# Performance work log

Hardware: AMD Instinct MI355X
Metric: run time of the kernel (lower is better)

## Reference

```python
import math
import jax, jax.numpy as jnp
import numpy as np

N, L, W = 64, 128, 256          # batch, num windows, window size
D, H, NL = 384, 8, 4            # d_model, heads, transformer layers
DFF = 1536
CH = [1, 4, 16, 64]             # conv channels (multiplier 4)
K = 7                            # conv kernel, pad 3, stride 1; pool k2 s2
LIN_IN = 64 * 32                # cnn_linear_size = 2048


def _pe(l, d):
    pos = np.arange(l)[:, None].astype(np.float32)
    i = np.arange(d // 2)[None, :].astype(np.float32)
    ang = pos / np.power(10000.0, 2.0 * i / d)
    pe = np.zeros((l, d), np.float32)
    pe[:, 0::2] = np.sin(ang)
    pe[:, 1::2] = np.cos(ang)
    return jnp.asarray(pe)


def _conv1d(x, w, b):
    y = jax.lax.conv_general_dilated(x, w, window_strides=(1,), padding=[(3, 3)],
                                     dimension_numbers=('NCH', 'OIH', 'NCH'))
    return y + b[None, :, None]


def _maxpool2(x):
    return jax.lax.reduce_window(x, -jnp.inf, jax.lax.max, (1, 1, 2), (1, 1, 2), 'VALID')


def _ln(x, g, b):
    m = x.mean(-1, keepdims=True)
    v = ((x - m) ** 2).mean(-1, keepdims=True)
    return (x - m) * jax.lax.rsqrt(v + 1e-5) * g + b


def setup_inputs() -> dict:
    key = jax.random.key(0)
    ks = iter(jax.random.split(key, 40))
    s = 0.02
    d = {'x': jax.random.normal(next(ks), (N, L, W), jnp.float32)}
    for i in range(3):
        d[f'conv_w{i}'] = jax.random.normal(next(ks), (CH[i + 1], CH[i], K), jnp.float32) * s
        d[f'conv_b{i}'] = jnp.zeros((CH[i + 1],), jnp.float32)
    d['embed_w'] = jax.random.normal(next(ks), (LIN_IN, D), jnp.float32) * s
    d['embed_b'] = jnp.zeros((D,), jnp.float32)
    for nm, sh in [('Wq', (NL, D, D)), ('Wk', (NL, D, D)), ('Wv', (NL, D, D)), ('Wo', (NL, D, D)),
                   ('W1', (NL, D, DFF)), ('W2', (NL, DFF, D))]:
        d[nm] = jax.random.normal(next(ks), sh, jnp.float32) * s
    for nm, sh in [('bq', (NL, D)), ('bk', (NL, D)), ('bv', (NL, D)), ('bo', (NL, D)),
                   ('b1', (NL, DFF)), ('b2', (NL, D))]:
        d[nm] = jnp.zeros(sh, jnp.float32)
    d['g1'] = jnp.ones((NL, D), jnp.float32); d['be1'] = jnp.zeros((NL, D), jnp.float32)
    d['g2'] = jnp.ones((NL, D), jnp.float32); d['be2'] = jnp.zeros((NL, D), jnp.float32)
    d['cls_w'] = jax.random.normal(next(ks), (D, 1), jnp.float32) * s
    d['cls_b'] = jnp.zeros((1,), jnp.float32)
    return d


def reference(x, conv_w0, conv_b0, conv_w1, conv_b1, conv_w2, conv_b2,
              embed_w, embed_b, Wq, bq, Wk, bk, Wv, bv, Wo, bo,
              W1, b1, W2, b2, g1, be1, g2, be2, cls_w, cls_b):
    n, l, w = x.shape
    # ---- CNN window encoder: each window -> d_model token ----
    h = x.reshape(n * l, 1, w)
    for cw, cb in ((conv_w0, conv_b0), (conv_w1, conv_b1), (conv_w2, conv_b2)):
        h = _maxpool2(jax.nn.relu(_conv1d(h, cw, cb)))
    h = h.reshape(n * l, -1)                      # (N*L, cnn_linear_size)
    h = jax.nn.relu(h @ embed_w + embed_b)        # (N*L, D)
    t = h.reshape(n, l, D) + _pe(l, D)
    # ---- transformer encoder (fast_transformers post-norm layers) ----
    E = D // H
    temp = 1.0 / math.sqrt(E)
    for i in range(Wq.shape[0]):
        q = (t @ Wq[i] + bq[i]).reshape(n, l, H, E)
        k = (t @ Wk[i] + bk[i]).reshape(n, l, H, E)
        v = (t @ Wv[i] + bv[i]).reshape(n, l, H, E)
        A = jax.nn.softmax(temp * jnp.einsum('nlhe,nshe->nhls', q, k), axis=-1)
        o = jnp.einsum('nhls,nshd->nlhd', A, v).reshape(n, l, D)
        t = _ln(t + o @ Wo[i] + bo[i], g1[i], be1[i])
        y = jax.nn.relu(t @ W1[i] + b1[i]) @ W2[i] + b2[i]
        t = _ln(t + y, g2[i], be2[i])
    # ---- classifier head: mean pool over windows -> logit ----
    return t.mean(axis=1) @ cls_w + cls_b          # (N, 1)
```

## Files before the change

kernel.cpp:

```cpp
#include <hip/hip_runtime.h>
#include <math.h>


typedef float f32x4 __attribute__((ext_vector_type(4)));
typedef short bf16x8 __attribute__((ext_vector_type(8)));
typedef short s16x4 __attribute__((ext_vector_type(4)));

__device__ __forceinline__ short f2bf(float f) {
    union { float f; unsigned u; } c; c.f = f;
    unsigned r = (c.u + 0x7FFFu + ((c.u >> 16) & 1u)) >> 16;
    return (short)r;
}
__device__ __forceinline__ float bf2f(short s) {
    union { unsigned u; float f; } c;
    c.u = ((unsigned)(unsigned short)s) << 16;
    return c.f;
}

__device__ __forceinline__ void gload_lds16(const void* g, void* l) {
    __builtin_amdgcn_global_load_lds(
        (const __attribute__((address_space(1))) unsigned int*)g,
        (__attribute__((address_space(3))) unsigned int*)l,
        16, 0, 0);
}

__global__ __launch_bounds__(256) void prep_kernel(
    const float* __restrict__ ew,
    const float* __restrict__ Wq, const float* __restrict__ Wk,
    const float* __restrict__ Wv, const float* __restrict__ Wo,
    const float* __restrict__ W1, const float* __restrict__ W2,
    const float* __restrict__ bq, const float* __restrict__ bk,
    const float* __restrict__ bv, const float* __restrict__ w2,
    short* __restrict__ ewT, short* __restrict__ WqkvT,
    short* __restrict__ WoT, short* __restrict__ W1T,
    short* __restrict__ W2T, float* __restrict__ pe,
    float* __restrict__ bqkv, short* __restrict__ w2T)
{
    __shared__ float tile[32][33];
    int id = blockIdx.x;
    int tid = threadIdx.x;
    int tx = tid & 31, ty = tid >> 5;

    const float* Wp;
    short* Wtp;
    int K, N, kb, nb;

    if (id < 768) {
        K = 2048; N = 384;
        kb = (id & 63) * 32; nb = (id >> 6) * 32;
        Wp = ew; Wtp = ewT;
    } else if (id < 2496) {
        int t = id - 768;
        int kbi = t % 12, nbi = (t / 12) % 12, z = t / 144;
        int layer = z / 3, which = z - layer * 3;
        K = 384; N = 384; kb = kbi * 32; nb = nbi * 32;
        Wp = (which == 0 ? Wq : (which == 1 ? Wk : Wv)) + (size_t)layer * 147456;
        Wtp = WqkvT + (size_t)layer * 442368 + (size_t)which * 147456;
    } else if (id < 3072) {
        int t = id - 2496;
        int kbi = t % 12, nbi = (t / 12) % 12, z = t / 144;
        K = 384; N = 384; kb = kbi * 32; nb = nbi * 32;
        Wp = Wo + (size_t)z * 147456; Wtp = WoT + (size_t)z * 147456;
    } else if (id < 5376) {
        int t = id - 3072;
        int kbi = t % 12, nbi = (t / 12) % 48, z = t / 576;
        K = 384; N = 1536; kb = kbi * 32; nb = nbi * 32;
        Wp = W1 + (size_t)z * 589824; Wtp = W1T + (size_t)z * 589824;
    } else if (id < 7680) {
        int t = id - 5376;
        int kbi = t % 48, nbi = (t / 48) % 12, z = t / 576;
        K = 1536; N = 384; kb = kbi * 32; nb = nbi * 32;
        Wp = W2 + (size_t)z * 589824; Wtp = W2T + (size_t)z * 589824;
    } else if (id < 7872) {
        int idx = (id - 7680) * 256 + tid;
        int l = idx / 384, d = idx - l * 384;
        int i2 = d >> 1;
        float ang = (float)l * expf(-(2.0f * (float)i2 / 384.0f) * 9.210340371976184f);
        pe[idx] = (d & 1) ? cosf(ang) : sinf(ang);
        return;
    } else if (id < 7890) {
        int idx = (id - 7872) * 256 + tid;
        int l = idx / 1152, j3 = idx - l * 1152;
        int which = j3 / 384, j = j3 - which * 384;
        const float* b = (which == 0 ? bq : (which == 1 ? bk : bv));
        bqkv[idx] = b[l * 384 + j];
        return;
    } else {
        int idx = (id - 7890) * 256 + tid;
        int c = idx >> 7, r = idx & 127;
        int pr = r >> 5, q = (r >> 3) & 3, j = r & 7;
        int ci = (q & 1) * 8 + j;
        int sft = 2 * pr + (q >> 1);
        w2T[idx] = (sft < 7) ? f2bf(w2[c * 112 + ci * 7 + sft]) : (short)0;
        return;
    }

    #pragma unroll
    for (int r = ty; r < 32; r += 8)
        tile[r][tx] = Wp[(size_t)(kb + r) * N + nb + tx];
    __syncthreads();
    #pragma unroll
    for (int r = ty; r < 32; r += 8)
        Wtp[(size_t)(nb + r) * K + kb + tx] = f2bf(tile[tx][r]);
}

__global__ __launch_bounds__(256, 4) void cnn_kernel(
    const float* __restrict__ x,
    const float* __restrict__ w0, const float* __restrict__ b0,
    const float* __restrict__ w1, const float* __restrict__ b1,
    const short* __restrict__ w2T, const float* __restrict__ b2,
    short* __restrict__ feat)
{
    __shared__ __align__(16) char smem[26880];
    float* xs  = (float*)smem;
    float* p0  = (float*)(smem + 4224);
    short* p1T = (short*)(smem + 13056);

    int tid = threadIdx.x;
    int w = tid >> 6, lane = tid & 63;
    size_t win = (size_t)blockIdx.x * 4 + w;
    int cq = lane >> 4, cl = lane & 15;

    float* xs_w = xs + w * 264;
    float* p0_w = p0 + w * 552;
    short* p1T_w = p1T + w * 1728;

    int ca = lane & 3;
    int cb = lane & 15, g = lane >> 4;
    float w0r[7], w1r[4][7];
    float b0r = b0[ca];
    float b1r = b1[cb];
    #pragma unroll
    for (int k = 0; k < 7; ++k) w0r[k] = w0[ca * 7 + k];
    #pragma unroll
    for (int ci = 0; ci < 4; ++ci)
        #pragma unroll
        for (int k = 0; k < 7; ++k) w1r[ci][k] = w1[(cb * 4 + ci) * 7 + k];

    {
        f32x4 v = *(const f32x4*)(x + win * 256 + lane * 4);
        *(f32x4*)&xs_w[4 + lane * 4] = v;
        if (lane < 2) *(f32x4*)&xs_w[lane * 260] = (f32x4){0.f, 0.f, 0.f, 0.f};
    }

    {
        int pa = lane >> 2;
        #pragma unroll
        for (int t2 = 0; t2 < 8; ++t2) {
            int pp = t2 * 16 + pa;
            float rv[9];
            #pragma unroll
            for (int u = 0; u < 9; ++u) rv[u] = xs_w[2 * pp + u + 1];
            float a0 = b0r, a1 = b0r;
            #pragma unroll
            for (int k = 0; k < 7; ++k) {
                a0 = fmaf(w0r[k], rv[k], a0);
                a1 = fmaf(w0r[k], rv[k + 1], a1);
            }
            p0_w[ca * 138 + pp + 3] = fmaxf(fmaxf(a0, a1), 0.f);
        }
        if (lane < 4) {
            p0_w[lane * 138 + 0] = 0.f;
            p0_w[lane * 138 + 1] = 0.f;
            p0_w[lane * 138 + 2] = 0.f;
            p0_w[lane * 138 + 131] = 0.f;
            p0_w[lane * 138 + 132] = 0.f;
            p0_w[lane * 138 + 133] = 0.f;
        }
    }

    #pragma unroll
    for (int cc = 0; cc < 4; ++cc) {
        int cci = (cc + g) & 3;
        int j0 = g * 32 + cci * 8;
        float acc[8];
        #pragma unroll
        for (int m = 0; m < 8; ++m) acc[m] = b1r;
        #pragma unroll
        for (int ci = 0; ci < 4; ++ci) {
            float rv[14];
            #pragma unroll
            for (int u = 0; u < 14; ++u) rv[u] = p0_w[ci * 138 + j0 + u];
            #pragma unroll
            for (int k = 0; k < 7; ++k) {
                float ww = w1r[ci][k];
                #pragma unroll
                for (int m = 0; m < 8; ++m) acc[m] = fmaf(ww, rv[m + k], acc[m]);
            }
        }
        int po = g * 16 + cci * 4;
        #pragma unroll
        for (int m = 0; m < 4; ++m)
            p1T_w[(3 + po + m) * 24 + cb] =
                f2bf(fmaxf(fmaxf(acc[2 * m], acc[2 * m + 1]), 0.f));
    }
    {
        int* pz = (int*)p1T_w;
        if (lane < 36) pz[lane] = 0;
        if (lane < 60) pz[804 + lane] = 0;
    }
    __syncthreads();

    f32x4 acc[4][4];
    #pragma unroll
    for (int v = 0; v < 4; ++v)
        #pragma unroll
        for (int mt = 0; mt < 4; ++mt)
            acc[v][mt] = (f32x4){0.f, 0.f, 0.f, 0.f};

    {
        const short* bpb = p1T + (w * 16 + cl + (cq >> 1)) * 24 + (cq & 1) * 8;
        #pragma unroll
        for (int pr = 0; pr < 4; ++pr) {
            bf16x8 bfr[4];
            #pragma unroll
            for (int v = 0; v < 4; ++v)
                bfr[v] = *(const bf16x8*)&bpb[v * 1728 + pr * 48];
            #pragma unroll
            for (int mt = 0; mt < 4; ++mt) {
                bf16x8 af = *(const bf16x8*)&w2T[(mt * 16 + cl) * 128 +
                                                 pr * 32 + cq * 8];
                #pragma unroll
                for (int v = 0; v < 4; ++v)
                    acc[v][mt] = __builtin_amdgcn_mfma_f32_16x16x32_bf16(
                        af, bfr[v], acc[v][mt], 0, 0, 0);
            }
        }
    }

    int iev = (w * 16 + cl) >> 1;
    #pragma unroll
    for (int v = 0; v < 4; ++v) {
        short* fp = feat + ((size_t)blockIdx.x * 4 + v) * 2048;
        #pragma unroll
        for (int mt = 0; mt < 4; ++mt) {
            #pragma unroll
            for (int rg = 0; rg < 4; ++rg) {
                float vv = acc[v][mt][rg];
                float v2 = __shfl_xor(vv, 1, 64);
                if ((cl & 1) == 0) {
                    int c = mt * 16 + cq * 4 + rg;
                    float pv = fmaxf(fmaxf(vv, v2) + b2[c], 0.f);
                    fp[c * 32 + iev] = f2bf(pv);
                }
            }
        }
    }
}

template <int EPI>
__global__ __launch_bounds__(256) void gemm_bf16(
    const short* __restrict__ A, const short* __restrict__ Bt,
    const float* __restrict__ bias, const float* __restrict__ resid,
    const float* __restrict__ pe, float* __restrict__ outF,
    short* __restrict__ outB, int M, int N, int K)
{
    __shared__ short As[2][128 * 64];
    __shared__ short Bs[2][64 * 64];
    int tid = threadIdx.x;
    int w = tid >> 6, lane = tid & 63;
    int wm = w >> 1, wn = w & 1;
    int m0 = blockIdx.y * 128, n0 = blockIdx.x * 64;

    int rl = lane >> 3, sl = lane & 7;
    int cb = sl ^ rl;
    const short* aptr[4];
    const short* bptr[2];
    int arow[4], brow[2];
    #pragma unroll
    for (int l = 0; l < 4; ++l) {
        arow[l] = l * 32 + w * 8;
        aptr[l] = A + (size_t)(m0 + arow[l] + rl) * K + cb * 8;
    }
    #pragma unroll
    for (int l = 0; l < 2; ++l) {
        brow[l] = l * 32 + w * 8;
        bptr[l] = Bt + (size_t)(n0 + brow[l] + rl) * K + cb * 8;
    }

    int cq = lane >> 4, cl = lane & 15;
    f32x4 acc[4][2];
    #pragma unroll
    for (int mt = 0; mt < 4; ++mt)
        #pragma unroll
        for (int nt = 0; nt < 2; ++nt)
            acc[mt][nt] = (f32x4){0.f, 0.f, 0.f, 0.f};

    #pragma unroll
    for (int l = 0; l < 4; ++l) { gload_lds16(aptr[l], &As[0][arow[l] * 64]); aptr[l] += 64; }
    #pragma unroll
    for (int l = 0; l < 2; ++l) { gload_lds16(bptr[l], &Bs[0][brow[l] * 64]); bptr[l] += 64; }
    __syncthreads();

    int nk = K >> 6;
    for (int k = 0; k < nk; ++k) {
        int cur = k & 1;
        if (k + 1 < nk) {
            #pragma unroll
            for (int l = 0; l < 4; ++l) { gload_lds16(aptr[l], &As[cur ^ 1][arow[l] * 64]); aptr[l] += 64; }
            #pragma unroll
            for (int l = 0; l < 2; ++l) { gload_lds16(bptr[l], &Bs[cur ^ 1][brow[l] * 64]); bptr[l] += 64; }
        }
        #pragma unroll
        for (int s = 0; s < 2; ++s) {
            bf16x8 afr[4], bfr[2];
            #pragma unroll
            for (int mt = 0; mt < 4; ++mt) {
                int r = wm * 64 + mt * 16 + cl;
                int slot = (s * 4 + cq) ^ (r & 7);
                afr[mt] = *(const bf16x8*)&As[cur][r * 64 + slot * 8];
            }
            #pragma unroll
            for (int nt = 0; nt < 2; ++nt) {
                int r = wn * 32 + nt * 16 + cl;
                int slot = (s * 4 + cq) ^ (r & 7);
                bfr[nt] = *(const bf16x8*)&Bs[cur][r * 64 + slot * 8];
            }
            #pragma unroll
            for (int mt = 0; mt < 4; ++mt)
                #pragma unroll
                for (int nt = 0; nt < 2; ++nt)
                    acc[mt][nt] = __builtin_amdgcn_mfma_f32_16x16x32_bf16(
                        afr[mt], bfr[nt], acc[mt][nt], 0, 0, 0);
        }
        __syncthreads();
    }

    #pragma unroll
    for (int mt = 0; mt < 4; ++mt) {
        #pragma unroll
        for (int nt = 0; nt < 2; ++nt) {
            int col = n0 + wn * 32 + nt * 16 + cl;
            float bb = bias[col];
            #pragma unroll
            for (int rg = 0; rg < 4; ++rg) {
                int row = m0 + wm * 64 + mt * 16 + cq * 4 + rg;
                float v = acc[mt][nt][rg] + bb;
                if (EPI & 1) v = fmaxf(v, 0.f);
                if (EPI & 4) v += pe[(row & 127) * 384 + col];
                if (EPI & 2) v += resid[(size_t)row * N + col];
                if (EPI & 8) outF[(size_t)row * N + col] = v;
                if (EPI & 16) outB[(size_t)row * N + col] = f2bf(v);
            }
        }
    }
}

template <int EPI>
__global__ __launch_bounds__(256) void gemm_bf16_wide(
    const short* __restrict__ A, const short* __restrict__ Bt,
    const float* __restrict__ bias, float* __restrict__ outF,
    short* __restrict__ outB, int M, int N, int K)
{
    __shared__ short As[2][128 * 32];
    __shared__ short Bs[2][128 * 32];
    int tid = threadIdx.x;
    int w = tid >> 6, lane = tid & 63;
    int wm = w >> 1, wn = w & 1;
    int m0 = blockIdx.y * 128, n0 = blockIdx.x * 128;

    int rl = lane >> 2, sl = lane & 3;
    int cb = sl ^ (rl & 3) ^ ((rl >> 2) & 3);
    const short* aptr[2];
    const short* bptr[2];
    int srow[2];
    #pragma unroll
    for (int l = 0; l < 2; ++l) {
        srow[l] = w * 32 + l * 16;
        aptr[l] = A + (size_t)(m0 + srow[l] + rl) * K + cb * 8;
        bptr[l] = Bt + (size_t)(n0 + srow[l] + rl) * K + cb * 8;
    }

    int cq = lane >> 4, cl = lane & 15;
    f32x4 acc[4][4];
    #pragma unroll
    for (int mt = 0; mt < 4; ++mt)
        #pragma unroll
        for (int nt = 0; nt < 4; ++nt)
            acc[mt][nt] = (f32x4){0.f, 0.f, 0.f, 0.f};

    #pragma unroll
    for (int l = 0; l < 2; ++l) {
        gload_lds16(aptr[l], &As[0][srow[l] * 32]);
        gload_lds16(bptr[l], &Bs[0][srow[l] * 32]);
        aptr[l] += 32; bptr[l] += 32;
    }
    __syncthreads();

    int nk = K >> 5;
    for (int k = 0; k < nk; ++k) {
        int cur = k & 1;
        if (k + 1 < nk) {
            #pragma unroll
            for (int l = 0; l < 2; ++l) {
                gload_lds16(aptr[l], &As[cur ^ 1][srow[l] * 32]);
                gload_lds16(bptr[l], &Bs[cur ^ 1][srow[l] * 32]);
                aptr[l] += 32; bptr[l] += 32;
            }
        }
        bf16x8 afr[4], bfr[4];
        #pragma unroll
        for (int mt = 0; mt < 4; ++mt) {
            int r = wm * 64 + mt * 16 + cl;
            int slot = cq ^ (r & 3) ^ ((r >> 2) & 3);
            afr[mt] = *(const bf16x8*)&As[cur][r * 32 + slot * 8];
        }
        #pragma unroll
        for (int nt = 0; nt < 4; ++nt) {
            int r = wn * 64 + nt * 16 + cl;
            int slot = cq ^ (r & 3) ^ ((r >> 2) & 3);
            bfr[nt] = *(const bf16x8*)&Bs[cur][r * 32 + slot * 8];
        }
        #pragma unroll
        for (int mt = 0; mt < 4; ++mt)
            #pragma unroll
            for (int nt = 0; nt < 4; ++nt)
                acc[mt][nt] = __builtin_amdgcn_mfma_f32_16x16x32_bf16(
                    afr[mt], bfr[nt], acc[mt][nt], 0, 0, 0);
        __syncthreads();
    }

    #pragma unroll
    for (int mt = 0; mt < 4; ++mt) {
        #pragma unroll
        for (int nt = 0; nt < 4; ++nt) {
            int col = n0 + wn * 64 + nt * 16 + cl;
            float bb = bias[col];
            #pragma unroll
            for (int rg = 0; rg < 4; ++rg) {
                int row = m0 + wm * 64 + mt * 16 + cq * 4 + rg;
                float v = acc[mt][nt][rg] + bb;
                if (EPI & 1) v = fmaxf(v, 0.f);
                if (EPI & 8) outF[(size_t)row * N + col] = v;
                if (EPI & 16) outB[(size_t)row * N + col] = f2bf(v);
            }
        }
    }
}

__global__ __launch_bounds__(512) void gemm_ln(
    const short* __restrict__ A, const short* __restrict__ Bt,
    const float* __restrict__ bias, const float* resid,
    const float* __restrict__ g, const float* __restrict__ be,
    float* t, short* __restrict__ tb, int K)
{
    __shared__ __align__(16) char smem[106496];
    short* As0 = (short*)smem;
    short* Bs0 = (short*)(smem + 8192);

    int tid = threadIdx.x;
    int w = tid >> 6, lane = tid & 63;
    int m0 = blockIdx.x * 32;
    int rl = lane >> 3, sl = lane & 7;
    int cb = sl ^ rl;

    const short* aptr = A + (size_t)(m0 + (w & 3) * 8 + rl) * K + cb * 8;
    const short* bptr[6];
    #pragma unroll
    for (int l = 0; l < 6; ++l)
        bptr[l] = Bt + (size_t)(w * 48 + l * 8 + rl) * K + cb * 8;

    int cq = lane >> 4, cl = lane & 15;
    f32x4 acc[2][3];
    #pragma unroll
    for (int mt = 0; mt < 2; ++mt)
        #pragma unroll
        for (int nt = 0; nt < 3; ++nt)
            acc[mt][nt] = (f32x4){0.f, 0.f, 0.f, 0.f};

    if (w < 4) { gload_lds16(aptr, &As0[(w * 8) * 64]); aptr += 64; }
    #pragma unroll
    for (int l = 0; l < 6; ++l) {
        gload_lds16(bptr[l], &Bs0[(w * 48 + l * 8) * 64]);
        bptr[l] += 64;
    }
    __syncthreads();

    int nk = K >> 6;
    for (int k = 0; k < nk; ++k) {
        int cur = k & 1;
        if (k + 1 < nk) {
            if (w < 4) { gload_lds16(aptr, &As0[(cur ^ 1) * 2048 + (w * 8) * 64]); aptr += 64; }
            #pragma unroll
            for (int l = 0; l < 6; ++l) {
                gload_lds16(bptr[l], &Bs0[(cur ^ 1) * 24576 + (w * 48 + l * 8) * 64]);
                bptr[l] += 64;
            }
        }
        const short* As = As0 + cur * 2048;
        const short* Bs = Bs0 + cur * 24576;
        #pragma unroll
        for (int s = 0; s < 2; ++s) {
            bf16x8 afr[2], bfr[3];
            #pragma unroll
            for (int mt = 0; mt < 2; ++mt) {
                int r = mt * 16 + cl;
                int slot = (s * 4 + cq) ^ (r & 7);
                afr[mt] = *(const bf16x8*)&As[r * 64 + slot * 8];
            }
            #pragma unroll
            for (int nt = 0; nt < 3; ++nt) {
                int r = w * 48 + nt * 16 + cl;
                int slot = (s * 4 + cq) ^ (r & 7);
                bfr[nt] = *(const bf16x8*)&Bs[r * 64 + slot * 8];
            }
            #pragma unroll
            for (int mt = 0; mt < 2; ++mt)
                #pragma unroll
                for (int nt = 0; nt < 3; ++nt)
                    acc[mt][nt] = __builtin_amdgcn_mfma_f32_16x16x32_bf16(
                        afr[mt], bfr[nt], acc[mt][nt], 0, 0, 0);
        }
        __syncthreads();
    }

    float* yb = (float*)smem;
    #pragma unroll
    for (int mt = 0; mt < 2; ++mt) {
        #pragma unroll
        for (int nt = 0; nt < 3; ++nt) {
            int col = w * 48 + nt * 16 + cl;
            float bb = bias[col];
            #pragma unroll
            for (int rg = 0; rg < 4; ++rg) {
                int rloc = mt * 16 + cq * 4 + rg;
                yb[rloc * 388 + col] =
                    acc[mt][nt][rg] + bb + resid[(size_t)(m0 + rloc) * 384 + col];
            }
        }
    }
    __syncthreads();

    int rloc = tid >> 4, sub = tid & 15;
    f32x4 vals[6];
    float s = 0.f, s2 = 0.f;
    #pragma unroll
    for (int m = 0; m < 6; ++m) {
        f32x4 vv = *(const f32x4*)&yb[rloc * 388 + m * 64 + sub * 4];
        vals[m] = vv;
        #pragma unroll
        for (int j = 0; j < 4; ++j) {
            s += vv[j];
            s2 = fmaf(vv[j], vv[j], s2);
        }
    }
    s += __shfl_xor(s, 1, 64);  s2 += __shfl_xor(s2, 1, 64);
    s += __shfl_xor(s, 2, 64);  s2 += __shfl_xor(s2, 2, 64);
    s += __shfl_xor(s, 4, 64);  s2 += __shfl_xor(s2, 4, 64);
    s += __shfl_xor(s, 8, 64);  s2 += __shfl_xor(s2, 8, 64);
    float mean = s * (1.f / 384.f);
    float var = s2 * (1.f / 384.f) - mean * mean;
    float inv = rsqrtf(var + 1e-5f);

    size_t ro = (size_t)(m0 + rloc) * 384;
    #pragma unroll
    for (int m = 0; m < 6; ++m) {
        int c0 = m * 64 + sub * 4;
        f32x4 gg = *(const f32x4*)&g[c0];
        f32x4 bb = *(const f32x4*)&be[c0];
        f32x4 ov;
        s16x4 ob2;
        #pragma unroll
        for (int j = 0; j < 4; ++j) {
            float v = (vals[m][j] - mean) * inv * gg[j] + bb[j];
            ov[j] = v;
            ob2[j] = f2bf(v);
        }
        *(f32x4*)&t[ro + c0] = ov;
        *(s16x4*)&tb[ro + c0] = ob2;
    }
}

__global__ __launch_bounds__(256) void attn_kernel(
    const short* __restrict__ qkv, short* __restrict__ o)
{
    __shared__ __align__(16) short lds[23936];
    short* Vt = lds;
    short* P  = lds + 6528;

    int tid = threadIdx.x;
    int w = tid >> 6, lane = tid & 63;
    int cq = lane >> 4, cl = lane & 15;
    int n = blockIdx.x >> 3, h = blockIdx.x & 7;
    size_t base = (size_t)n * 147456 + (size_t)h * 48;
    const short* qp = qkv + base;
    const short* kp = qkv + base + 384;
    const short* vp = qkv + base + 768;

    {
        int key = tid >> 1, half = tid & 1;
        const short* vsrc = vp + (size_t)key * 1152 + half * 24;
        #pragma unroll
        for (int e4 = 0; e4 < 6; ++e4) {
            s16x4 vv = *(const s16x4*)(vsrc + e4 * 4);
            int e0 = half * 24 + e4 * 4;
            Vt[(e0 + 0) * 136 + key] = vv[0];
            Vt[(e0 + 1) * 136 + key] = vv[1];
            Vt[(e0 + 2) * 136 + key] = vv[2];
            Vt[(e0 + 3) * 136 + key] = vv[3];
        }
    }

    const bf16x8 zf = (bf16x8){0, 0, 0, 0, 0, 0, 0, 0};
    bf16x8 qf[2][2];
    #pragma unroll
    for (int mt = 0; mt < 2; ++mt) {
        const short* qrow = qp + (size_t)(w * 32 + mt * 16 + cl) * 1152;
        qf[mt][0] = *(const bf16x8*)(qrow + cq * 8);
        qf[mt][1] = (cq < 2) ? *(const bf16x8*)(qrow + 32 + cq * 8) : zf;
    }

    f32x4 sacc[2][8];
    #pragma unroll
    for (int mt = 0; mt < 2; ++mt)
        #pragma unroll
        for (int kt = 0; kt < 8; ++kt)
            sacc[mt][kt] = (f32x4){0.f, 0.f, 0.f, 0.f};

    #pragma unroll
    for (int kt = 0; kt < 8; ++kt) {
        const short* krow = kp + (size_t)(kt * 16 + cl) * 1152;
        bf16x8 kf0 = *(const bf16x8*)(krow + cq * 8);
        bf16x8 kf1 = (cq < 2) ? *(const bf16x8*)(krow + 32 + cq * 8) : zf;
        #pragma unroll
        for (int mt = 0; mt < 2; ++mt) {
            sacc[mt][kt] = __builtin_amdgcn_mfma_f32_16x16x32_bf16(
                qf[mt][0], kf0, sacc[mt][kt], 0, 0, 0);
            sacc[mt][kt] = __builtin_amdgcn_mfma_f32_16x16x32_bf16(
                qf[mt][1], kf1, sacc[mt][kt], 0, 0, 0);
        }
    }
    __syncthreads();

    const float temp = 0.14433756729740643f;
    short* Pw = P + w * 4352;
    float denom[2][4];
    #pragma unroll
    for (int mt = 0; mt < 2; ++mt) {
        #pragma unroll
        for (int rg = 0; rg < 4; ++rg) {
            float m0 = sacc[mt][0][rg];
            #pragma unroll
            for (int kt = 1; kt < 8; ++kt) m0 = fmaxf(m0, sacc[mt][kt][rg]);
            m0 = fmaxf(m0, __shfl_xor(m0, 1, 64));
            m0 = fmaxf(m0, __shfl_xor(m0, 2, 64));
            m0 = fmaxf(m0, __shfl_xor(m0, 4, 64));
            m0 = fmaxf(m0, __shfl_xor(m0, 8, 64));
            int row = mt * 16 + cq * 4 + rg;
            float se = 0.f;
            #pragma unroll
            for (int kt = 0; kt < 8; ++kt) {
                float p = __expf(temp * (sacc[mt][kt][rg] - m0));
                se += p;
                Pw[row * 136 + kt * 16 + cl] = f2bf(p);
            }
            se += __shfl_xor(se, 1, 64);
            se += __shfl_xor(se, 2, 64);
            se += __shfl_xor(se, 4, 64);
            se += __shfl_xor(se, 8, 64);
            denom[mt][rg] = se;
        }
    }

    f32x4 oacc[2][3];
    #pragma unroll
    for (int mt = 0; mt < 2; ++mt)
        #pragma unroll
        for (int nt = 0; nt < 3; ++nt)
            oacc[mt][nt] = (f32x4){0.f, 0.f, 0.f, 0.f};

    #pragma unroll
    for (int ks = 0; ks < 4; ++ks) {
        bf16x8 paf[2];
        #pragma unroll
        for (int mt = 0; mt < 2; ++mt)
            paf[mt] = *(const bf16x8*)&Pw[(mt * 16 + cl) * 136 + ks * 32 + cq * 8];
        #pragma unroll
        for (int nt = 0; nt < 3; ++nt) {
            bf16x8 vf = *(const bf16x8*)&Vt[(nt * 16 + cl) * 136 + ks * 32 + cq * 8];
            #pragma unroll
            for (int mt = 0; mt < 2; ++mt)
                oacc[mt][nt] = __builtin_amdgcn_mfma_f32_16x16x32_bf16(
                    paf[mt], vf, oacc[mt][nt], 0, 0, 0);
        }
    }

    #pragma unroll
    for (int mt = 0; mt < 2; ++mt) {
        #pragma unroll
        for (int rg = 0; rg < 4; ++rg) {
            float inv = 1.f / denom[mt][rg];
            int qrow = w * 32 + mt * 16 + cq * 4 + rg;
            short* op = o + ((size_t)n * 128 + qrow) * 384 + h * 48;
            #pragma unroll
            for (int nt = 0; nt < 3; ++nt)
                op[nt * 16 + cl] = f2bf(oacc[mt][nt][rg] * inv);
        }
    }
}

__global__ __launch_bounds__(384) void head_kernel(
    const float* __restrict__ t, const float* __restrict__ cls_w,
    const float* __restrict__ cls_b, float* __restrict__ out)
{
    int n = blockIdx.x, d = threadIdx.x;
    float s = 0.f;
    for (int l = 0; l < 128; ++l) s += t[((size_t)n * 128 + l) * 384 + d];
    float p = s * (1.f / 128.f) * cls_w[d];
    #pragma unroll
    for (int off = 32; off > 0; off >>= 1) p += __shfl_xor(p, off, 64);
    __shared__ float red[6];
    if ((threadIdx.x & 63) == 0) red[threadIdx.x >> 6] = p;
    __syncthreads();
    if (threadIdx.x == 0) {
        float tot = red[0] + red[1] + red[2] + red[3] + red[4] + red[5];
        out[n] = tot + cls_b[0];
    }
}

extern "C" void kernel_launch(void* const* d_in, const int* in_sizes, int n_in,
                              void* d_out, int out_size, void* d_ws, size_t ws_size,
                              hipStream_t stream) {
    (void)n_in; (void)out_size; (void)ws_size;
    const float* x   = (const float*)d_in[0];
    const float* cw0 = (const float*)d_in[1];
    const float* cb0 = (const float*)d_in[2];
    const float* cw1 = (const float*)d_in[3];
    const float* cb1 = (const float*)d_in[4];
    const float* cw2 = (const float*)d_in[5];
    const float* cb2 = (const float*)d_in[6];
    const float* ew  = (const float*)d_in[7];
    const float* eb  = (const float*)d_in[8];
    bool dict_order = (in_sizes[10] == 589824);
    const float *Wq, *Wk, *Wv, *Wo, *W1, *W2, *bq, *bk, *bv, *bo, *b1, *b2;
    if (dict_order) {
        Wq = (const float*)d_in[9];  Wk = (const float*)d_in[10];
        Wv = (const float*)d_in[11]; Wo = (const float*)d_in[12];
        W1 = (const float*)d_in[13]; W2 = (const float*)d_in[14];
        bq = (const float*)d_in[15]; bk = (const float*)d_in[16];
        bv = (const float*)d_in[17]; bo = (const float*)d_in[18];
        b1 = (const float*)d_in[19]; b2 = (const float*)d_in[20];
    } else {
        Wq = (const float*)d_in[9];  bq = (const float*)d_in[10];
        Wk = (const float*)d_in[11]; bk = (const float*)d_in[12];
        Wv = (const float*)d_in[13]; bv = (const float*)d_in[14];
        Wo = (const float*)d_in[15]; bo = (const float*)d_in[16];
        W1 = (const float*)d_in[17]; b1 = (const float*)d_in[18];
        W2 = (const float*)d_in[19]; b2 = (const float*)d_in[20];
    }
    const float* g1  = (const float*)d_in[21];
    const float* be1 = (const float*)d_in[22];
    const float* g2  = (const float*)d_in[23];
    const float* be2 = (const float*)d_in[24];
    const float* clw = (const float*)d_in[25];
    const float* clb = (const float*)d_in[26];

    char* wp = (char*)d_ws;
    float* pe    = (float*)wp; wp += 196608;
    short* featb = (short*)wp; wp += 33554432;
    float* t     = (float*)wp; wp += 12582912;
    short* tb    = (short*)wp; wp += 6291456;
    short* qkvb  = (short*)wp; wp += 18874368;
    short* ob    = (short*)wp; wp += 6291456;
    short* ewT   = (short*)wp; wp += 1572864;
    short* WqkvT = (short*)wp; wp += 3538944;
    short* WoT   = (short*)wp; wp += 1179648;
    short* W1T   = (short*)wp; wp += 4718592;
    short* W2T   = (short*)wp; wp += 4718592;
    float* bqkv  = (float*)wp; wp += 18432;
    short* w2T   = (short*)wp; wp += 16384;
    short* hb    = featb;

    const int ROWS = 8192;

    prep_kernel<<<7922, 256, 0, stream>>>(ew, Wq, Wk, Wv, Wo, W1, W2,
                                          bq, bk, bv, cw2,
                                          ewT, WqkvT, WoT, W1T, W2T,
                                          pe, bqkv, w2T);
    cnn_kernel<<<2048, 256, 0, stream>>>(x, cw0, cb0, cw1, cb1, w2T, cb2, featb);

    gemm_bf16<29><<<dim3(6, 64), 256, 0, stream>>>(featb, ewT, eb, nullptr, pe,
                                                   t, tb, ROWS, 384, 2048);
    for (int i = 0; i < 4; ++i) {
        const short* WqkvTi = WqkvT + (size_t)i * 442368;
        const short* WoTi = WoT + (size_t)i * 147456;
        const short* W1Ti = W1T + (size_t)i * 589824;
        const short* W2Ti = W2T + (size_t)i * 589824;
        gemm_bf16_wide<16><<<dim3(9, 64), 256, 0, stream>>>(tb, WqkvTi,
            bqkv + i * 1152, nullptr, qkvb, ROWS, 1152, 384);
        attn_kernel<<<512, 256, 0, stream>>>(qkvb, ob);
        gemm_ln<<<256, 512, 0, stream>>>(ob, WoTi, bo + i * 384, t,
            g1 + i * 384, be1 + i * 384, t, tb, 384);
        gemm_bf16_wide<17><<<dim3(12, 64), 256, 0, stream>>>(tb, W1Ti,
            b1 + i * 1536, nullptr, hb, ROWS, 1536, 384);
        gemm_ln<<<256, 512, 0, stream>>>(hb, W2Ti, b2 + i * 384, t,
            g2 + i * 384, be2 + i * 384, t, tb, 1536);
    }
    head_kernel<<<64, 384, 0, stream>>>(t, clw, clb, (float*)d_out);
}
```

Measured before the change: 601.8 us.

## Fuse QKV projection GEMM into per-head attention kernel

Replaces the separate QKV GEMM and attention kernels with one kernel per (batch, head) block. Each block computes the 128x144 Q/K/V slice with a double-buffered LDS GEMM and writes Q, K and transposed V straight into shared memory before running the attention. This removes the qkv round trip through global memory and one launch per layer. The cost is that each block re-reads the full 128x384 activation tile for every head, and the kernel uses about 75KB of LDS, which may reduce occupancy.

```diff
diff --git a/kernel.cpp b/kernel.cpp
--- a/kernel.cpp
+++ b/kernel.cpp
@@ -571,43 +571,135 @@
     }
 }
 
-__global__ __launch_bounds__(256) void attn_kernel(
-    const short* __restrict__ qkv, short* __restrict__ o)
+__global__ __launch_bounds__(256) void qkvattn_kernel(
+    const short* __restrict__ A, const short* __restrict__ Bt,
+    const float* __restrict__ bias, short* __restrict__ o)
 {
-    __shared__ __align__(16) short lds[23936];
-    short* Vt = lds;
-    short* P  = lds + 6528;
+    __shared__ __align__(16) char smem[76544];
+    short* As0 = (short*)smem;
+    short* Bs0 = (short*)(smem + 32768);
+    short* Qs  = (short*)smem;
+    short* Ks  = (short*)(smem + 14336);
+    short* Vt  = (short*)(smem + 28672);
+    short* P   = (short*)(smem + 41728);
 
     int tid = threadIdx.x;
     int w = tid >> 6, lane = tid & 63;
     int cq = lane >> 4, cl = lane & 15;
     int n = blockIdx.x >> 3, h = blockIdx.x & 7;
-    size_t base = (size_t)n * 147456 + (size_t)h * 48;
-    const short* qp = qkv + base;
-    const short* kp = qkv + base + 384;
-    const short* vp = qkv + base + 768;
-
-    {
-        int key = tid >> 1, half = tid & 1;
-        const short* vsrc = vp + (size_t)key * 1152 + half * 24;
-        #pragma unroll
-        for (int e4 = 0; e4 < 6; ++e4) {
-            s16x4 vv = *(const s16x4*)(vsrc + e4 * 4);
-            int e0 = half * 24 + e4 * 4;
-            Vt[(e0 + 0) * 136 + key] = vv[0];
-            Vt[(e0 + 1) * 136 + key] = vv[1];
-            Vt[(e0 + 2) * 136 + key] = vv[2];
-            Vt[(e0 + 3) * 136 + key] = vv[3];
-        }
-    }
+    int m0 = n * 128;
+
+    int rl = lane >> 3, sl = lane & 7;
+    int cb = sl ^ rl;
+    const short* aptr[4];
+    int arow[4];
+    #pragma unroll
+    for (int l = 0; l < 4; ++l) {
+        arow[l] = l * 32 + w * 8;
+        aptr[l] = A + (size_t)(m0 + arow[l] + rl) * 384 + cb * 8;
+    }
+    const short* bptr[5];
+    int brow[5];
+    #pragma unroll
+    for (int l = 0; l < 5; ++l) {
+        brow[l] = (l < 4) ? (l * 32 + w * 8) : (128 + w * 8);
+        int r = brow[l] + rl;
+        int g0 = (r >= 96) ? 2 : ((r >= 48) ? 1 : 0);
+        int loc = r - g0 * 48;
+        bptr[l] = Bt + (size_t)(g0 * 384 + h * 48 + loc) * 384 + cb * 8;
+    }
+
+    f32x4 acc[2][9];
+    #pragma unroll
+    for (int mt = 0; mt < 2; ++mt)
+        #pragma unroll
+        for (int nt = 0; nt < 9; ++nt)
+            acc[mt][nt] = (f32x4){0.f, 0.f, 0.f, 0.f};
+
+    #pragma unroll
+    for (int l = 0; l < 4; ++l) { gload_lds16(aptr[l], &As0[arow[l] * 64]); aptr[l] += 64; }
+    #pragma unroll
+    for (int l = 0; l < 5; ++l) {
+        if (l < 4 || w < 2) { gload_lds16(bptr[l], &Bs0[brow[l] * 64]); }
+        bptr[l] += 64;
+    }
+    __syncthreads();
+
+    for (int k = 0; k < 6; ++k) {
+        int cur = k & 1;
+        if (k + 1 < 6) {
+            #pragma unroll
+            for (int l = 0; l < 4; ++l) {
+                gload_lds16(aptr[l], &As0[(cur ^ 1) * 8192 + arow[l] * 64]);
+                aptr[l] += 64;
+            }
+            #pragma unroll
+            for (int l = 0; l < 5; ++l) {
+                if (l < 4 || w < 2)
+                    gload_lds16(bptr[l], &Bs0[(cur ^ 1) * 9216 + brow[l] * 64]);
+                bptr[l] += 64;
+            }
+        }
+        const short* Asb = As0 + cur * 8192;
+        const short* Bsb = Bs0 + cur * 9216;
+        #pragma unroll
+        for (int s = 0; s < 2; ++s) {
+            bf16x8 afr[2], bfr[9];
+            #pragma unroll
+            for (int mt = 0; mt < 2; ++mt) {
+                int r = w * 32 + mt * 16 + cl;
+                int slot = (s * 4 + cq) ^ (r & 7);
+                afr[mt] = *(const bf16x8*)&Asb[r * 64 + slot * 8];
+            }
+            #pragma unroll
+            for (int nt = 0; nt < 9; ++nt) {
+                int r = nt * 16 + cl;
+                int slot = (s * 4 + cq) ^ (r & 7);
+                bfr[nt] = *(const bf16x8*)&Bsb[r * 64 + slot * 8];
+            }
+            #pragma unroll
+            for (int mt = 0; mt < 2; ++mt)
+                #pragma unroll
+                for (int nt = 0; nt < 9; ++nt)
+                    acc[mt][nt] = __builtin_amdgcn_mfma_f32_16x16x32_bf16(
+                        afr[mt], bfr[nt], acc[mt][nt], 0, 0, 0);
+        }
+        __syncthreads();
+    }
+
+    const float* bh = bias + h * 48;
+    #pragma unroll
+    for (int mt = 0; mt < 2; ++mt) {
+        #pragma unroll
+        for (int nt = 0; nt < 9; ++nt) {
+            int grp = nt / 3;
+            int col = (nt - grp * 3) * 16 + cl;
+            float bb = bh[grp * 384 + col];
+            if (grp == 2) {
+                int row0 = w * 32 + mt * 16 + cq * 4;
+                s16x4 pv;
+                #pragma unroll
+                for (int rg = 0; rg < 4; ++rg) pv[rg] = f2bf(acc[mt][nt][rg] + bb);
+                *(s16x4*)&Vt[col * 136 + row0] = pv;
+            } else {
+                short* dst = (grp == 0) ? Qs : Ks;
+                #pragma unroll
+                for (int rg = 0; rg < 4; ++rg) {
+                    int row = w * 32 + mt * 16 + cq * 4 + rg;
+                    dst[row * 56 + col] = f2bf(acc[mt][nt][rg] + bb);
+                }
+            }
+        }
+    }
+    __syncthreads();
 
     const bf16x8 zf = (bf16x8){0, 0, 0, 0, 0, 0, 0, 0};
     bf16x8 qf[2][2];
     #pragma unroll
     for (int mt = 0; mt < 2; ++mt) {
-        const short* qrow = qp + (size_t)(w * 32 + mt * 16 + cl) * 1152;
-        qf[mt][0] = *(const bf16x8*)(qrow + cq * 8);
-        qf[mt][1] = (cq < 2) ? *(const bf16x8*)(qrow + 32 + cq * 8) : zf;
+        int r = w * 32 + mt * 16 + cl;
+        qf[mt][0] = *(const bf16x8*)&Qs[r * 56 + cq * 8];
+        qf[mt][1] = (cq < 2) ? *(const bf16x8*)&Qs[r * 56 + 32 + cq * 8] : zf;
     }
 
     f32x4 sacc[2][8];
@@ -619,9 +711,9 @@
 
     #pragma unroll
     for (int kt = 0; kt < 8; ++kt) {
-        const short* krow = kp + (size_t)(kt * 16 + cl) * 1152;
-        bf16x8 kf0 = *(const bf16x8*)(krow + cq * 8);
-        bf16x8 kf1 = (cq < 2) ? *(const bf16x8*)(krow + 32 + cq * 8) : zf;
+        int r = kt * 16 + cl;
+        bf16x8 kf0 = *(const bf16x8*)&Ks[r * 56 + cq * 8];
+        bf16x8 kf1 = (cq < 2) ? *(const bf16x8*)&Ks[r * 56 + 32 + cq * 8] : zf;
         #pragma unroll
         for (int mt = 0; mt < 2; ++mt) {
             sacc[mt][kt] = __builtin_amdgcn_mfma_f32_16x16x32_bf16(
@@ -630,7 +722,6 @@
                 qf[mt][1], kf1, sacc[mt][kt], 0, 0, 0);
         }
     }
-    __syncthreads();
 
     const float temp = 0.14433756729740643f;
     short* Pw = P + w * 4352;
@@ -639,18 +730,18 @@
     for (int mt = 0; mt < 2; ++mt) {
         #pragma unroll
         for (int rg = 0; rg < 4; ++rg) {
-            float m0 = sacc[mt][0][rg];
-            #pragma unroll
-            for (int kt = 1; kt < 8; ++kt) m0 = fmaxf(m0, sacc[mt][kt][rg]);
-            m0 = fmaxf(m0, __shfl_xor(m0, 1, 64));
-            m0 = fmaxf(m0, __shfl_xor(m0, 2, 64));
-            m0 = fmaxf(m0, __shfl_xor(m0, 4, 64));
-            m0 = fmaxf(m0, __shfl_xor(m0, 8, 64));
+            float mx = sacc[mt][0][rg];
+            #pragma unroll
+            for (int kt = 1; kt < 8; ++kt) mx = fmaxf(mx, sacc[mt][kt][rg]);
+            mx = fmaxf(mx, __shfl_xor(mx, 1, 64));
+            mx = fmaxf(mx, __shfl_xor(mx, 2, 64));
+            mx = fmaxf(mx, __shfl_xor(mx, 4, 64));
+            mx = fmaxf(mx, __shfl_xor(mx, 8, 64));
             int row = mt * 16 + cq * 4 + rg;
             float se = 0.f;
             #pragma unroll
             for (int kt = 0; kt < 8; ++kt) {
-                float p = __expf(temp * (sacc[mt][kt][rg] - m0));
+                float p = __expf(temp * (sacc[mt][kt][rg] - mx));
                 se += p;
                 Pw[row * 136 + kt * 16 + cl] = f2bf(p);
             }
@@ -770,6 +861,7 @@
     float* bqkv  = (float*)wp; wp += 18432;
     short* w2T   = (short*)wp; wp += 16384;
     short* hb    = featb;
+    (void)qkvb;
 
     const int ROWS = 8192;
 
@@ -786,9 +878,7 @@
         const short* WoTi = WoT + (size_t)i * 147456;
         const short* W1Ti = W1T + (size_t)i * 589824;
         const short* W2Ti = W2T + (size_t)i * 589824;
-        gemm_bf16_wide<16><<<dim3(9, 64), 256, 0, stream>>>(tb, WqkvTi,
-            bqkv + i * 1152, nullptr, qkvb, ROWS, 1152, 384);
-        attn_kernel<<<512, 256, 0, stream>>>(qkvb, ob);
+        qkvattn_kernel<<<512, 256, 0, stream>>>(tb, WqkvTi, bqkv + i * 1152, ob);
         gemm_ln<<<256, 512, 0, stream>>>(ob, WoTi, bo + i * 384, t,
             g1 + i * 384, be1 + i * 384, t, tb, 384);
         gemm_bf16_wide<17><<<dim3(12, 64), 256, 0, stream>>>(tb, W1Ti,
```

Measured after the change: 569.7 us (median of 2 runs). 5.3% less time.
